# Kernel tuning notes

Measured on AMD Instinct MI355X. Metric: run time of the kernel, lower is better.

The kernel has to match this reference:

```python
import jax, jax.numpy as jnp
import numpy as np


def _layer_norm(x, w, b, eps=1e-5):
    mu = jnp.mean(x, axis=-1, keepdims=True)
    var = jnp.mean((x - mu) ** 2, axis=-1, keepdims=True)
    return (x - mu) * jax.lax.rsqrt(var + eps) * w + b


def setup_inputs() -> dict:
    key = jax.random.key(0)
    ks = jax.random.split(key, 6)
    B, S, E, H = 4, 4096, 1024, 16
    dk = E // H            # = n_qubits_transformer = 64
    NQF = 64               # n_qubits_ffn
    x = jax.random.normal(ks[0], (B, S, E), jnp.float32)
    attn_q_params = jax.random.normal(ks[1], (dk, 3), jnp.float32)   # torch.randn init
    out_proj_w = jax.random.normal(ks[2], (E, E), jnp.float32) / np.float32(np.sqrt(E))
    out_proj_b = jnp.zeros((E,), jnp.float32)
    ffn_q_params = jax.random.normal(ks[3], (NQF, 3), jnp.float32)
    ffn_lin_w = jax.random.normal(ks[4], (E, NQF), jnp.float32) / np.float32(np.sqrt(NQF))
    ffn_lin_b = jnp.zeros((E,), jnp.float32)
    return {
        'x': x,
        'attn_q_params': attn_q_params,
        'out_proj_w': out_proj_w,
        'out_proj_b': out_proj_b,
        'ffn_q_params': ffn_q_params,
        'ffn_lin_w': ffn_lin_w,
        'ffn_lin_b': ffn_lin_b,
        'norm1_w': jnp.ones((E,), jnp.float32),
        'norm1_b': jnp.zeros((E,), jnp.float32),
        'norm2_w': jnp.ones((E,), jnp.float32),
        'norm2_b': jnp.zeros((E,), jnp.float32),
    }


def reference(x, attn_q_params, out_proj_w, out_proj_b,
              ffn_q_params, ffn_lin_w, ffn_lin_b,
              norm1_w, norm1_b, norm2_w, norm2_b):
    # Closed form: <Z> = cos(x + a) * cos(b); Rz does not affect <Z>.
    B, S, E = x.shape
    dk = attn_q_params.shape[0]
    H = E // dk
    # ---- quantum multi-head attention (shared QHead params across heads) ----
    heads = x.reshape(B, S, H, dk)                                   # bshd
    z = jnp.cos(heads + attn_q_params[:, 0]) * jnp.cos(attn_q_params[:, 1])
    attn_out = z.reshape(B, S, E) @ out_proj_w.T + out_proj_b
    x1 = _layer_norm(x + attn_out, norm1_w, norm1_b)                 # dropout = identity (eval)
    # ---- quantum feed-forward: encoder uses first n_qubits_ffn features ----
    nq = ffn_q_params.shape[0]
    q = jnp.cos(x1[..., :nq] + ffn_q_params[:, 0]) * jnp.cos(ffn_q_params[:, 1])
    ffn_out = q @ ffn_lin_w.T + ffn_lin_b
    return _layer_norm(x1 + ffn_out, norm2_w, norm2_b)
```

## Files before the change

### kernel.cpp

```cpp
#include <hip/hip_runtime.h>
#include <math.h>

typedef __attribute__((ext_vector_type(8))) short short8;
typedef __attribute__((ext_vector_type(4))) float f32x4;
typedef unsigned short u16;

#define DEV static __device__ __forceinline__

DEV u16 f2bf(float f) {
  union { float f; unsigned u; } v; v.f = f;
  unsigned r = v.u + 0x7FFFu + ((v.u >> 16) & 1u);
  return (u16)(r >> 16);
}
DEV float bf2f(u16 u) {
  union { unsigned u; float f; } v; v.u = ((unsigned)u) << 16;
  return v.f;
}

__global__ __launch_bounds__(256) void k_conv(const float* __restrict__ W,
                                              const float* __restrict__ Wf,
                                              u16* __restrict__ Wb,
                                              u16* __restrict__ Wfb) {
  int i = (blockIdx.x * 256 + threadIdx.x) * 4;
  const int NW = 1024 * 1024;
  if (i < NW) {
    float4 v = *(const float4*)(W + i);
    ushort4 o = {f2bf(v.x), f2bf(v.y), f2bf(v.z), f2bf(v.w)};
    *(ushort4*)(Wb + i) = o;
  } else {
    int j = i - NW;
    float4 v = *(const float4*)(Wf + j);
    ushort4 o = {f2bf(v.x), f2bf(v.y), f2bf(v.z), f2bf(v.w)};
    *(ushort4*)(Wfb + j) = o;
  }
}

__global__ __launch_bounds__(256) void k_zenc(const float* __restrict__ x,
                                              const float* __restrict__ qp,
                                              u16* __restrict__ z) {
  __shared__ float a0[64], c1[64];
  int t = threadIdx.x;
  if (t < 64) { a0[t] = qp[t * 3]; c1[t] = cosf(qp[t * 3 + 1]); }
  __syncthreads();
  size_t i = ((size_t)blockIdx.x * 256 + t) * 4;
  float4 xv = *(const float4*)(x + i);
  int d = (int)(i & 63);
  ushort4 o;
  o.x = f2bf(cosf(xv.x + a0[d + 0]) * c1[d + 0]);
  o.y = f2bf(cosf(xv.y + a0[d + 1]) * c1[d + 1]);
  o.z = f2bf(cosf(xv.z + a0[d + 2]) * c1[d + 2]);
  o.w = f2bf(cosf(xv.w + a0[d + 3]) * c1[d + 3]);
  *(ushort4*)(z + i) = o;
}

__global__ __launch_bounds__(256) void k_gemm(const u16* __restrict__ Z,
                                              const u16* __restrict__ Wb,
                                              const float* __restrict__ x,
                                              const float* __restrict__ bias,
                                              float* __restrict__ Y) {
  constexpr int K = 1024, N = 1024;
  __shared__ __attribute__((aligned(16))) u16 As[2][128 * 32];
  __shared__ __attribute__((aligned(16))) u16 Bs[2][128 * 32];
  int bid = blockIdx.x;
  int wg = (bid & 7) * 128 + (bid >> 3);
  int mt = wg >> 3, nt = wg & 7;
  int m0 = mt * 128, n0 = nt * 128;
  int t = threadIdx.x, lane = t & 63, wv = t >> 6;
  int wr = wv >> 1, wc = wv & 1;

  int srow = t >> 2;
  int scol = (t & 3) * 8;
  const u16* gA = Z + (size_t)(m0 + srow) * K + scol;
  const u16* gB = Wb + (size_t)(n0 + srow) * K + scol;
  int lbase = wv * 512;

  f32x4 acc[4][4];
#pragma unroll
  for (int i = 0; i < 4; ++i)
#pragma unroll
    for (int j = 0; j < 4; ++j) acc[i][j] = (f32x4){0.f, 0.f, 0.f, 0.f};

  auto stage = [&](int buf, int kt) {
    const u16* ga = gA + kt * 32;
    const u16* gb = gB + kt * 32;
#pragma unroll
    for (int j = 0; j < 2; ++j) {
      __builtin_amdgcn_global_load_lds(
          (const __attribute__((address_space(1))) unsigned int*)(ga + (size_t)j * 64 * K),
          (__attribute__((address_space(3))) unsigned int*)&As[buf][j * 2048 + lbase],
          16, 0, 0);
      __builtin_amdgcn_global_load_lds(
          (const __attribute__((address_space(1))) unsigned int*)(gb + (size_t)j * 64 * K),
          (__attribute__((address_space(3))) unsigned int*)&Bs[buf][j * 2048 + lbase],
          16, 0, 0);
    }
  };

  stage(0, 0);
  int kof = (lane >> 4) * 8;
  int arow = wr * 64 + (lane & 15);
  int brow = wc * 64 + (lane & 15);
  int cur = 0;
  for (int kt = 0; kt < K / 32; ++kt) {
    __syncthreads();
    if (kt + 1 < K / 32) stage(cur ^ 1, kt + 1);
    short8 av[4], bv[4];
#pragma unroll
    for (int mi = 0; mi < 4; ++mi)
      av[mi] = *(const short8*)&As[cur][(arow + mi * 16) * 32 + kof];
#pragma unroll
    for (int ni = 0; ni < 4; ++ni)
      bv[ni] = *(const short8*)&Bs[cur][(brow + ni * 16) * 32 + kof];
#pragma unroll
    for (int mi = 0; mi < 4; ++mi)
#pragma unroll
      for (int ni = 0; ni < 4; ++ni)
        acc[mi][ni] = __builtin_amdgcn_mfma_f32_16x16x32_bf16(av[mi], bv[ni], acc[mi][ni], 0, 0, 0);
    cur ^= 1;
  }
  int r0 = m0 + wr * 64 + (lane >> 4) * 4;
  int c0 = n0 + wc * 64 + (lane & 15);
#pragma unroll
  for (int mi = 0; mi < 4; ++mi) {
#pragma unroll
    for (int ni = 0; ni < 4; ++ni) {
      int col = c0 + ni * 16;
      float bcol = bias[col];
#pragma unroll
      for (int r = 0; r < 4; ++r) {
        size_t idx = (size_t)(r0 + mi * 16 + r) * N + col;
        Y[idx] = acc[mi][ni][r] + x[idx] + bcol;
      }
    }
  }
}

__global__ __launch_bounds__(256) void k_ln1(const float* __restrict__ Y,
                                             const float* __restrict__ w1,
                                             const float* __restrict__ b1,
                                             const float* __restrict__ fqp,
                                             u16* __restrict__ X1,
                                             u16* __restrict__ Q) {
  int t = threadIdx.x, lane = t & 63, wv = t >> 6;
  int row = blockIdx.x * 4 + wv;
  const float* yr = Y + (size_t)row * 1024;
  float4 v[4];
  float s = 0.f, s2 = 0.f;
#pragma unroll
  for (int j = 0; j < 4; ++j) {
    v[j] = *(const float4*)(yr + j * 256 + lane * 4);
    s += v[j].x + v[j].y + v[j].z + v[j].w;
    s2 += v[j].x * v[j].x + v[j].y * v[j].y + v[j].z * v[j].z + v[j].w * v[j].w;
  }
#pragma unroll
  for (int m = 1; m < 64; m <<= 1) { s += __shfl_xor(s, m, 64); s2 += __shfl_xor(s2, m, 64); }
  float mu = s * (1.f / 1024.f);
  float var = s2 * (1.f / 1024.f) - mu * mu;
  float rs = rsqrtf(var + 1e-5f);
  float q0[4];
#pragma unroll
  for (int j = 0; j < 4; ++j) {
    int col = j * 256 + lane * 4;
    float4 wv4 = *(const float4*)(w1 + col);
    float4 bv4 = *(const float4*)(b1 + col);
    float o0 = (v[j].x - mu) * rs * wv4.x + bv4.x;
    float o1 = (v[j].y - mu) * rs * wv4.y + bv4.y;
    float o2 = (v[j].z - mu) * rs * wv4.z + bv4.z;
    float o3 = (v[j].w - mu) * rs * wv4.w + bv4.w;
    ushort4 o = {f2bf(o0), f2bf(o1), f2bf(o2), f2bf(o3)};
    *(ushort4*)(X1 + (size_t)row * 1024 + col) = o;
    if (j == 0) { q0[0] = o0; q0[1] = o1; q0[2] = o2; q0[3] = o3; }
  }
  if (lane < 16) {
    ushort4 qo;
    u16* qs = (u16*)&qo;
#pragma unroll
    for (int c = 0; c < 4; ++c) {
      int col = lane * 4 + c;
      qs[c] = f2bf(cosf(q0[c] + fqp[col * 3]) * cosf(fqp[col * 3 + 1]));
    }
    *(ushort4*)(Q + (size_t)row * 64 + lane * 4) = qo;
  }
}

__global__ __launch_bounds__(256) void k_ffn(const u16* __restrict__ X1,
                                             const u16* __restrict__ Q,
                                             const u16* __restrict__ Wfb,
                                             const float* __restrict__ fb,
                                             const float* __restrict__ w2,
                                             const float* __restrict__ b2,
                                             float* __restrict__ out) {
  __shared__ float t2[16][1024];
  int t = threadIdx.x, lane = t & 63, wv = t >> 6;
  int m0 = blockIdx.x * 16;
  int kof = (lane >> 4) * 8;
  const short8 a0v = *(const short8*)&Q[(size_t)(m0 + (lane & 15)) * 64 + kof];
  const short8 a1v = *(const short8*)&Q[(size_t)(m0 + (lane & 15)) * 64 + 32 + kof];
  int nbase = wv * 256;
#pragma unroll
  for (int ni = 0; ni < 16; ++ni) {
    int n = nbase + ni * 16 + (lane & 15);
    short8 b0 = *(const short8*)&Wfb[(size_t)n * 64 + kof];
    short8 b1 = *(const short8*)&Wfb[(size_t)n * 64 + 32 + kof];
    f32x4 acc = (f32x4){0.f, 0.f, 0.f, 0.f};
    acc = __builtin_amdgcn_mfma_f32_16x16x32_bf16(a0v, b0, acc, 0, 0, 0);
    acc = __builtin_amdgcn_mfma_f32_16x16x32_bf16(a1v, b1, acc, 0, 0, 0);
#pragma unroll
    for (int r = 0; r < 4; ++r) t2[(lane >> 4) * 4 + r][n] = acc[r];
  }
  __syncthreads();
  for (int rr = 0; rr < 4; ++rr) {
    int row = wv * 4 + rr;
    size_t grow = (size_t)(m0 + row) * 1024;
    float vv[16];
    float s = 0.f, s2 = 0.f;
#pragma unroll
    for (int j = 0; j < 16; ++j) {
      int col = j * 64 + lane;
      float val = bf2f(X1[grow + col]) + t2[row][col] + fb[col];
      vv[j] = val; s += val; s2 += val * val;
    }
#pragma unroll
    for (int m = 1; m < 64; m <<= 1) { s += __shfl_xor(s, m, 64); s2 += __shfl_xor(s2, m, 64); }
    float mu = s * (1.f / 1024.f);
    float var = s2 * (1.f / 1024.f) - mu * mu;
    float rs = rsqrtf(var + 1e-5f);
#pragma unroll
    for (int j = 0; j < 16; ++j) {
      int col = j * 64 + lane;
      out[grow + col] = (vv[j] - mu) * rs * w2[col] + b2[col];
    }
  }
}

extern "C" void kernel_launch(void* const* d_in, const int* in_sizes, int n_in,
                              void* d_out, int out_size, void* d_ws, size_t ws_size,
                              hipStream_t stream) {
  const float* x   = (const float*)d_in[0];
  const float* aqp = (const float*)d_in[1];
  const float* opw = (const float*)d_in[2];
  const float* opb = (const float*)d_in[3];
  const float* fqp = (const float*)d_in[4];
  const float* flw = (const float*)d_in[5];
  const float* flb = (const float*)d_in[6];
  const float* n1w = (const float*)d_in[7];
  const float* n1b = (const float*)d_in[8];
  const float* n2w = (const float*)d_in[9];
  const float* n2b = (const float*)d_in[10];
  float* Y = (float*)d_out;

  char* ws = (char*)d_ws;
  u16* zbuf = (u16*)(ws + 0);
  u16* Wb   = (u16*)(ws + 33554432);
  u16* Wfb  = (u16*)(ws + 35651584);
  u16* Qb   = (u16*)(ws + 35782656);

  k_conv<<<1088, 256, 0, stream>>>(opw, flw, Wb, Wfb);
  k_zenc<<<16384, 256, 0, stream>>>(x, aqp, zbuf);
  k_gemm<<<1024, 256, 0, stream>>>(zbuf, Wb, x, opb, Y);
  k_ln1<<<4096, 256, 0, stream>>>(Y, n1w, n1b, fqp, zbuf , Qb);
  k_ffn<<<1024, 256, 0, stream>>>(zbuf, Qb, Wfb, flb, n2w, n2b, Y);
}
```

Before: 138.9 us.

## Fuse output-projection GEMM with LayerNorm1 using full-row tiles per block

Replaces the separate GEMM and LayerNorm1 kernels with one kernel. Each 512-thread block computes a 64-row by full-1024-column output tile, so row statistics can be reduced in registers and shared memory. It then writes bf16 X1 and the FFN encoder inputs directly, removing the fp32 intermediate write and re-read. The cost is one large block per CU with about 130KB of LDS for the double-buffered B tile and 128 accumulator registers per lane. That leaves low occupancy, weaker latency hiding, and a whole-block synchronization on every k-step.

```diff
diff --git a/kernel.cpp b/kernel.cpp
--- a/kernel.cpp
+++ b/kernel.cpp
@@ -53,133 +53,143 @@
   *(ushort4*)(z + i) = o;
 }
 
-__global__ __launch_bounds__(256) void k_gemm(const u16* __restrict__ Z,
-                                              const u16* __restrict__ Wb,
-                                              const float* __restrict__ x,
-                                              const float* __restrict__ bias,
-                                              float* __restrict__ Y) {
-  constexpr int K = 1024, N = 1024;
-  __shared__ __attribute__((aligned(16))) u16 As[2][128 * 32];
-  __shared__ __attribute__((aligned(16))) u16 Bs[2][128 * 32];
-  int bid = blockIdx.x;
-  int wg = (bid & 7) * 128 + (bid >> 3);
-  int mt = wg >> 3, nt = wg & 7;
-  int m0 = mt * 128, n0 = nt * 128;
+__global__ __launch_bounds__(512) void k_gemm_ln1(
+    const u16* __restrict__ Z, const u16* __restrict__ Wb,
+    const float* __restrict__ x, const float* __restrict__ opb,
+    const float* __restrict__ w1, const float* __restrict__ b1,
+    const float* __restrict__ fqp,
+    u16* __restrict__ X1, u16* __restrict__ Q) {
+  constexpr int K = 1024;
+  __shared__ __attribute__((aligned(16))) u16 As[2][64 * 32];
+  __shared__ __attribute__((aligned(16))) u16 Bs[2][1024 * 32];
+  __shared__ float redS[64][8];
+  __shared__ float redQ[64][8];
+  __shared__ float muF[64], rsF[64];
+
   int t = threadIdx.x, lane = t & 63, wv = t >> 6;
-  int wr = wv >> 1, wc = wv & 1;
-
-  int srow = t >> 2;
-  int scol = (t & 3) * 8;
-  const u16* gA = Z + (size_t)(m0 + srow) * K + scol;
-  const u16* gB = Wb + (size_t)(n0 + srow) * K + scol;
-  int lbase = wv * 512;
-
-  f32x4 acc[4][4];
-#pragma unroll
-  for (int i = 0; i < 4; ++i)
-#pragma unroll
-    for (int j = 0; j < 4; ++j) acc[i][j] = (f32x4){0.f, 0.f, 0.f, 0.f};
+  int m0 = blockIdx.x * 64;
+
+  const u16* gA = Z + (size_t)(m0 + (t >> 2)) * K + (t & 3) * 8;
+  const u16* gB = Wb + (size_t)(t >> 2) * K + (t & 3) * 8;
 
   auto stage = [&](int buf, int kt) {
-    const u16* ga = gA + kt * 32;
-    const u16* gb = gB + kt * 32;
-#pragma unroll
-    for (int j = 0; j < 2; ++j) {
+    int ko = kt * 32;
+    if (t < 256) {
       __builtin_amdgcn_global_load_lds(
-          (const __attribute__((address_space(1))) unsigned int*)(ga + (size_t)j * 64 * K),
-          (__attribute__((address_space(3))) unsigned int*)&As[buf][j * 2048 + lbase],
+          (const __attribute__((address_space(1))) unsigned int*)(gA + ko),
+          (__attribute__((address_space(3))) unsigned int*)&As[buf][wv * 512],
           16, 0, 0);
+    }
+#pragma unroll
+    for (int j = 0; j < 8; ++j) {
       __builtin_amdgcn_global_load_lds(
-          (const __attribute__((address_space(1))) unsigned int*)(gb + (size_t)j * 64 * K),
-          (__attribute__((address_space(3))) unsigned int*)&Bs[buf][j * 2048 + lbase],
+          (const __attribute__((address_space(1))) unsigned int*)(gB + (size_t)j * 128 * K + ko),
+          (__attribute__((address_space(3))) unsigned int*)&Bs[buf][j * 4096 + wv * 512],
           16, 0, 0);
     }
   };
 
+  f32x4 acc[4][8];
+#pragma unroll
+  for (int m = 0; m < 4; ++m)
+#pragma unroll
+    for (int n = 0; n < 8; ++n) acc[m][n] = (f32x4){0.f, 0.f, 0.f, 0.f};
+
   stage(0, 0);
+  int cur = 0;
   int kof = (lane >> 4) * 8;
-  int arow = wr * 64 + (lane & 15);
-  int brow = wc * 64 + (lane & 15);
-  int cur = 0;
+  int cl = lane & 15;
   for (int kt = 0; kt < K / 32; ++kt) {
     __syncthreads();
     if (kt + 1 < K / 32) stage(cur ^ 1, kt + 1);
-    short8 av[4], bv[4];
-#pragma unroll
-    for (int mi = 0; mi < 4; ++mi)
-      av[mi] = *(const short8*)&As[cur][(arow + mi * 16) * 32 + kof];
-#pragma unroll
-    for (int ni = 0; ni < 4; ++ni)
-      bv[ni] = *(const short8*)&Bs[cur][(brow + ni * 16) * 32 + kof];
-#pragma unroll
-    for (int mi = 0; mi < 4; ++mi)
-#pragma unroll
-      for (int ni = 0; ni < 4; ++ni)
-        acc[mi][ni] = __builtin_amdgcn_mfma_f32_16x16x32_bf16(av[mi], bv[ni], acc[mi][ni], 0, 0, 0);
+    short8 av[4], bv[8];
+#pragma unroll
+    for (int m = 0; m < 4; ++m)
+      av[m] = *(const short8*)&As[cur][(m * 16 + cl) * 32 + kof];
+#pragma unroll
+    for (int n = 0; n < 8; ++n)
+      bv[n] = *(const short8*)&Bs[cur][(wv * 128 + n * 16 + cl) * 32 + kof];
+#pragma unroll
+    for (int m = 0; m < 4; ++m)
+#pragma unroll
+      for (int n = 0; n < 8; ++n)
+        acc[m][n] = __builtin_amdgcn_mfma_f32_16x16x32_bf16(av[m], bv[n], acc[m][n], 0, 0, 0);
     cur ^= 1;
   }
-  int r0 = m0 + wr * 64 + (lane >> 4) * 4;
-  int c0 = n0 + wc * 64 + (lane & 15);
-#pragma unroll
-  for (int mi = 0; mi < 4; ++mi) {
-#pragma unroll
-    for (int ni = 0; ni < 4; ++ni) {
-      int col = c0 + ni * 16;
-      float bcol = bias[col];
+
+  int rbase = (lane >> 4) * 4;
+  float w1c[8], b1c[8];
+#pragma unroll
+  for (int n = 0; n < 8; ++n) {
+    int col = wv * 128 + n * 16 + cl;
+    w1c[n] = w1[col];
+    b1c[n] = b1[col];
+  }
+  float rowS[16], rowQ2[16];
+#pragma unroll
+  for (int i = 0; i < 16; ++i) { rowS[i] = 0.f; rowQ2[i] = 0.f; }
+#pragma unroll
+  for (int m = 0; m < 4; ++m) {
+#pragma unroll
+    for (int n = 0; n < 8; ++n) {
+      int col = wv * 128 + n * 16 + cl;
+      float bias = opb[col];
 #pragma unroll
       for (int r = 0; r < 4; ++r) {
-        size_t idx = (size_t)(r0 + mi * 16 + r) * N + col;
-        Y[idx] = acc[mi][ni][r] + x[idx] + bcol;
+        int row = m * 16 + rbase + r;
+        float v = acc[m][n][r] + x[(size_t)(m0 + row) * 1024 + col] + bias;
+        acc[m][n][r] = v;
+        rowS[m * 4 + r] += v;
+        rowQ2[m * 4 + r] += v * v;
       }
     }
   }
-}
-
-__global__ __launch_bounds__(256) void k_ln1(const float* __restrict__ Y,
-                                             const float* __restrict__ w1,
-                                             const float* __restrict__ b1,
-                                             const float* __restrict__ fqp,
-                                             u16* __restrict__ X1,
-                                             u16* __restrict__ Q) {
-  int t = threadIdx.x, lane = t & 63, wv = t >> 6;
-  int row = blockIdx.x * 4 + wv;
-  const float* yr = Y + (size_t)row * 1024;
-  float4 v[4];
-  float s = 0.f, s2 = 0.f;
-#pragma unroll
-  for (int j = 0; j < 4; ++j) {
-    v[j] = *(const float4*)(yr + j * 256 + lane * 4);
-    s += v[j].x + v[j].y + v[j].z + v[j].w;
-    s2 += v[j].x * v[j].x + v[j].y * v[j].y + v[j].z * v[j].z + v[j].w * v[j].w;
-  }
-#pragma unroll
-  for (int m = 1; m < 64; m <<= 1) { s += __shfl_xor(s, m, 64); s2 += __shfl_xor(s2, m, 64); }
-  float mu = s * (1.f / 1024.f);
-  float var = s2 * (1.f / 1024.f) - mu * mu;
-  float rs = rsqrtf(var + 1e-5f);
-  float q0[4];
-#pragma unroll
-  for (int j = 0; j < 4; ++j) {
-    int col = j * 256 + lane * 4;
-    float4 wv4 = *(const float4*)(w1 + col);
-    float4 bv4 = *(const float4*)(b1 + col);
-    float o0 = (v[j].x - mu) * rs * wv4.x + bv4.x;
-    float o1 = (v[j].y - mu) * rs * wv4.y + bv4.y;
-    float o2 = (v[j].z - mu) * rs * wv4.z + bv4.z;
-    float o3 = (v[j].w - mu) * rs * wv4.w + bv4.w;
-    ushort4 o = {f2bf(o0), f2bf(o1), f2bf(o2), f2bf(o3)};
-    *(ushort4*)(X1 + (size_t)row * 1024 + col) = o;
-    if (j == 0) { q0[0] = o0; q0[1] = o1; q0[2] = o2; q0[3] = o3; }
-  }
-  if (lane < 16) {
-    ushort4 qo;
-    u16* qs = (u16*)&qo;
-#pragma unroll
-    for (int c = 0; c < 4; ++c) {
-      int col = lane * 4 + c;
-      qs[c] = f2bf(cosf(q0[c] + fqp[col * 3]) * cosf(fqp[col * 3 + 1]));
-    }
-    *(ushort4*)(Q + (size_t)row * 64 + lane * 4) = qo;
+#pragma unroll
+  for (int i = 0; i < 16; ++i) {
+#pragma unroll
+    for (int msk = 1; msk < 16; msk <<= 1) {
+      rowS[i] += __shfl_xor(rowS[i], msk, 64);
+      rowQ2[i] += __shfl_xor(rowQ2[i], msk, 64);
+    }
+  }
+  if (cl == 0) {
+#pragma unroll
+    for (int m = 0; m < 4; ++m)
+#pragma unroll
+      for (int r = 0; r < 4; ++r) {
+        int row = m * 16 + rbase + r;
+        redS[row][wv] = rowS[m * 4 + r];
+        redQ[row][wv] = rowQ2[m * 4 + r];
+      }
+  }
+  __syncthreads();
+  if (t < 64) {
+    float s = 0.f, q = 0.f;
+#pragma unroll
+    for (int w = 0; w < 8; ++w) { s += redS[t][w]; q += redQ[t][w]; }
+    float mu = s * (1.f / 1024.f);
+    float var = q * (1.f / 1024.f) - mu * mu;
+    muF[t] = mu;
+    rsF[t] = rsqrtf(var + 1e-5f);
+  }
+  __syncthreads();
+#pragma unroll
+  for (int m = 0; m < 4; ++m) {
+#pragma unroll
+    for (int r = 0; r < 4; ++r) {
+      int row = m * 16 + rbase + r;
+      float mu = muF[row], rs = rsF[row];
+#pragma unroll
+      for (int n = 0; n < 8; ++n) {
+        int col = wv * 128 + n * 16 + cl;
+        float x1 = (acc[m][n][r] - mu) * rs * w1c[n] + b1c[n];
+        X1[(size_t)(m0 + row) * 1024 + col] = f2bf(x1);
+        if (wv == 0 && n < 4) {
+          float qv = cosf(x1 + fqp[col * 3]) * cosf(fqp[col * 3 + 1]);
+          Q[(size_t)(m0 + row) * 64 + col] = f2bf(qv);
+        }
+      }
+    }
   }
 }
 
@@ -247,7 +257,7 @@
   const float* n1b = (const float*)d_in[8];
   const float* n2w = (const float*)d_in[9];
   const float* n2b = (const float*)d_in[10];
-  float* Y = (float*)d_out;
+  float* out = (float*)d_out;
 
   char* ws = (char*)d_ws;
   u16* zbuf = (u16*)(ws + 0);
@@ -257,7 +267,7 @@
 
   k_conv<<<1088, 256, 0, stream>>>(opw, flw, Wb, Wfb);
   k_zenc<<<16384, 256, 0, stream>>>(x, aqp, zbuf);
-  k_gemm<<<1024, 256, 0, stream>>>(zbuf, Wb, x, opb, Y);
-  k_ln1<<<4096, 256, 0, stream>>>(Y, n1w, n1b, fqp, zbuf , Qb);
-  k_ffn<<<1024, 256, 0, stream>>>(zbuf, Qb, Wfb, flb, n2w, n2b, Y);
-}
+  k_gemm_ln1<<<256, 512, 0, stream>>>(zbuf, Wb, x, opb, n1w, n1b, fqp,
+                                      zbuf , Qb);
+  k_ffn<<<1024, 256, 0, stream>>>(zbuf, Qb, Wfb, flb, n2w, n2b, out);
+}
```

Result: slower. 449.8 us (+223.9%).

## Fuse LayerNorm row statistics into GEMM epilogue, store bf16 intermediate, swizzle LDS

Applied to the files above, without the earlier changes.

The GEMM epilogue now reduces per-row sums and sums of squares across lanes and writes partial stats per column tile. It stores the pre-norm activations as bf16 instead of fp32. The LN1 kernel then reads only the bf16 row plus 16 partial stats, which halves its traffic and drops its reduction pass. The GEMM also XOR-swizzles the LDS k-block layout to cut bank conflicts. This adds epilogue shuffles and an extra bf16 rounding of the pre-norm values before normalization.

```diff
diff --git a/kernel.cpp b/kernel.cpp
--- a/kernel.cpp
+++ b/kernel.cpp
@@ -56,8 +56,9 @@
 __global__ __launch_bounds__(256) void k_gemm(const u16* __restrict__ Z,
                                               const u16* __restrict__ Wb,
                                               const float* __restrict__ x,
-                                              const float* __restrict__ bias,
-                                              float* __restrict__ Y) {
+                                              const float* __restrict__ opb,
+                                              u16* __restrict__ Ybf,
+                                              float2* __restrict__ stats) {
   constexpr int K = 1024, N = 1024;
   __shared__ __attribute__((aligned(16))) u16 As[2][128 * 32];
   __shared__ __attribute__((aligned(16))) u16 Bs[2][128 * 32];
@@ -68,10 +69,9 @@
   int t = threadIdx.x, lane = t & 63, wv = t >> 6;
   int wr = wv >> 1, wc = wv & 1;
 
-  int srow = t >> 2;
-  int scol = (t & 3) * 8;
-  const u16* gA = Z + (size_t)(m0 + srow) * K + scol;
-  const u16* gB = Wb + (size_t)(n0 + srow) * K + scol;
+  int kb_log = (t & 3) ^ ((t >> 3) & 3);
+  const u16* gA = Z + (size_t)(m0 + (t >> 2)) * K + kb_log * 8;
+  const u16* gB = Wb + (size_t)(n0 + (t >> 2)) * K + kb_log * 8;
   int lbase = wv * 512;
 
   f32x4 acc[4][4];
@@ -97,9 +97,10 @@
   };
 
   stage(0, 0);
-  int kof = (lane >> 4) * 8;
-  int arow = wr * 64 + (lane & 15);
-  int brow = wc * 64 + (lane & 15);
+  int cl = lane & 15;
+  int kofs = ((lane >> 4) ^ ((lane >> 1) & 3)) * 8;
+  int arow = wr * 64 + cl;
+  int brow = wc * 64 + cl;
   int cur = 0;
   for (int kt = 0; kt < K / 32; ++kt) {
     __syncthreads();
@@ -107,10 +108,10 @@
     short8 av[4], bv[4];
 #pragma unroll
     for (int mi = 0; mi < 4; ++mi)
-      av[mi] = *(const short8*)&As[cur][(arow + mi * 16) * 32 + kof];
+      av[mi] = *(const short8*)&As[cur][(arow + mi * 16) * 32 + kofs];
 #pragma unroll
     for (int ni = 0; ni < 4; ++ni)
-      bv[ni] = *(const short8*)&Bs[cur][(brow + ni * 16) * 32 + kof];
+      bv[ni] = *(const short8*)&Bs[cur][(brow + ni * 16) * 32 + kofs];
 #pragma unroll
     for (int mi = 0; mi < 4; ++mi)
 #pragma unroll
@@ -118,24 +119,50 @@
         acc[mi][ni] = __builtin_amdgcn_mfma_f32_16x16x32_bf16(av[mi], bv[ni], acc[mi][ni], 0, 0, 0);
     cur ^= 1;
   }
+
   int r0 = m0 + wr * 64 + (lane >> 4) * 4;
-  int c0 = n0 + wc * 64 + (lane & 15);
+  int c0 = n0 + wc * 64 + cl;
+  float rowS[16], rowQ2[16];
+#pragma unroll
+  for (int i = 0; i < 16; ++i) { rowS[i] = 0.f; rowQ2[i] = 0.f; }
 #pragma unroll
   for (int mi = 0; mi < 4; ++mi) {
 #pragma unroll
     for (int ni = 0; ni < 4; ++ni) {
       int col = c0 + ni * 16;
-      float bcol = bias[col];
+      float bcol = opb[col];
 #pragma unroll
       for (int r = 0; r < 4; ++r) {
         size_t idx = (size_t)(r0 + mi * 16 + r) * N + col;
-        Y[idx] = acc[mi][ni][r] + x[idx] + bcol;
+        float v = acc[mi][ni][r] + x[idx] + bcol;
+        Ybf[idx] = f2bf(v);
+        rowS[mi * 4 + r] += v;
+        rowQ2[mi * 4 + r] += v * v;
       }
     }
   }
-}
-
-__global__ __launch_bounds__(256) void k_ln1(const float* __restrict__ Y,
+#pragma unroll
+  for (int i = 0; i < 16; ++i) {
+#pragma unroll
+    for (int msk = 1; msk < 16; msk <<= 1) {
+      rowS[i] += __shfl_xor(rowS[i], msk, 64);
+      rowQ2[i] += __shfl_xor(rowQ2[i], msk, 64);
+    }
+  }
+  if (cl == 0) {
+#pragma unroll
+    for (int mi = 0; mi < 4; ++mi)
+#pragma unroll
+      for (int r = 0; r < 4; ++r) {
+        int rg = r0 + mi * 16 + r;
+        stats[(size_t)rg * 16 + nt * 2 + wc] =
+            make_float2(rowS[mi * 4 + r], rowQ2[mi * 4 + r]);
+      }
+  }
+}
+
+__global__ __launch_bounds__(256) void k_ln1(const u16* __restrict__ Ybf,
+                                             const float2* __restrict__ stats,
                                              const float* __restrict__ w1,
                                              const float* __restrict__ b1,
                                              const float* __restrict__ fqp,
@@ -143,43 +170,45 @@
                                              u16* __restrict__ Q) {
   int t = threadIdx.x, lane = t & 63, wv = t >> 6;
   int row = blockIdx.x * 4 + wv;
-  const float* yr = Y + (size_t)row * 1024;
-  float4 v[4];
-  float s = 0.f, s2 = 0.f;
-#pragma unroll
-  for (int j = 0; j < 4; ++j) {
-    v[j] = *(const float4*)(yr + j * 256 + lane * 4);
-    s += v[j].x + v[j].y + v[j].z + v[j].w;
-    s2 += v[j].x * v[j].x + v[j].y * v[j].y + v[j].z * v[j].z + v[j].w * v[j].w;
-  }
-#pragma unroll
-  for (int m = 1; m < 64; m <<= 1) { s += __shfl_xor(s, m, 64); s2 += __shfl_xor(s2, m, 64); }
+  float2 st = stats[(size_t)row * 16 + (lane & 15)];
+  float s = st.x, s2 = st.y;
+#pragma unroll
+  for (int msk = 1; msk < 16; msk <<= 1) {
+    s += __shfl_xor(s, msk, 64);
+    s2 += __shfl_xor(s2, msk, 64);
+  }
   float mu = s * (1.f / 1024.f);
   float var = s2 * (1.f / 1024.f) - mu * mu;
   float rs = rsqrtf(var + 1e-5f);
-  float q0[4];
-#pragma unroll
-  for (int j = 0; j < 4; ++j) {
-    int col = j * 256 + lane * 4;
-    float4 wv4 = *(const float4*)(w1 + col);
-    float4 bv4 = *(const float4*)(b1 + col);
-    float o0 = (v[j].x - mu) * rs * wv4.x + bv4.x;
-    float o1 = (v[j].y - mu) * rs * wv4.y + bv4.y;
-    float o2 = (v[j].z - mu) * rs * wv4.z + bv4.z;
-    float o3 = (v[j].w - mu) * rs * wv4.w + bv4.w;
-    ushort4 o = {f2bf(o0), f2bf(o1), f2bf(o2), f2bf(o3)};
-    *(ushort4*)(X1 + (size_t)row * 1024 + col) = o;
-    if (j == 0) { q0[0] = o0; q0[1] = o1; q0[2] = o2; q0[3] = o3; }
-  }
-  if (lane < 16) {
-    ushort4 qo;
-    u16* qs = (u16*)&qo;
-#pragma unroll
-    for (int c = 0; c < 4; ++c) {
-      int col = lane * 4 + c;
-      qs[c] = f2bf(cosf(q0[c] + fqp[col * 3]) * cosf(fqp[col * 3 + 1]));
-    }
-    *(ushort4*)(Q + (size_t)row * 64 + lane * 4) = qo;
+
+  size_t base = (size_t)row * 1024 + lane * 16;
+  short8 y0 = *(const short8*)&Ybf[base];
+  short8 y1 = *(const short8*)&Ybf[base + 8];
+  float x1v[16];
+#pragma unroll
+  for (int j = 0; j < 8; ++j) x1v[j] = bf2f((u16)y0[j]);
+#pragma unroll
+  for (int j = 0; j < 8; ++j) x1v[8 + j] = bf2f((u16)y1[j]);
+  int col0 = lane * 16;
+#pragma unroll
+  for (int j = 0; j < 16; ++j)
+    x1v[j] = (x1v[j] - mu) * rs * w1[col0 + j] + b1[col0 + j];
+  short8 o0, o1;
+#pragma unroll
+  for (int j = 0; j < 8; ++j) { o0[j] = (short)f2bf(x1v[j]); o1[j] = (short)f2bf(x1v[8 + j]); }
+  *(short8*)&X1[base] = o0;
+  *(short8*)&X1[base + 8] = o1;
+
+  if (lane < 4) {
+    short8 q0, q1;
+#pragma unroll
+    for (int j = 0; j < 16; ++j) {
+      int c = col0 + j;
+      float qv = cosf(x1v[j] + fqp[c * 3]) * cosf(fqp[c * 3 + 1]);
+      if (j < 8) q0[j] = (short)f2bf(qv); else q1[j - 8] = (short)f2bf(qv);
+    }
+    *(short8*)&Q[(size_t)row * 64 + col0] = q0;
+    *(short8*)&Q[(size_t)row * 64 + col0 + 8] = q1;
   }
 }
 
@@ -247,7 +276,7 @@
   const float* n1b = (const float*)d_in[8];
   const float* n2w = (const float*)d_in[9];
   const float* n2b = (const float*)d_in[10];
-  float* Y = (float*)d_out;
+  float* out = (float*)d_out;
 
   char* ws = (char*)d_ws;
   u16* zbuf = (u16*)(ws + 0);
@@ -255,9 +284,12 @@
   u16* Wfb  = (u16*)(ws + 35651584);
   u16* Qb   = (u16*)(ws + 35782656);
 
+  u16* Ybf = (u16*)d_out;
+  float2* stats = (float2*)((char*)d_out + 33554432);
+
   k_conv<<<1088, 256, 0, stream>>>(opw, flw, Wb, Wfb);
   k_zenc<<<16384, 256, 0, stream>>>(x, aqp, zbuf);
-  k_gemm<<<1024, 256, 0, stream>>>(zbuf, Wb, x, opb, Y);
-  k_ln1<<<4096, 256, 0, stream>>>(Y, n1w, n1b, fqp, zbuf , Qb);
-  k_ffn<<<1024, 256, 0, stream>>>(zbuf, Qb, Wfb, flb, n2w, n2b, Y);
-}
+  k_gemm<<<1024, 256, 0, stream>>>(zbuf, Wb, x, opb, Ybf, stats);
+  k_ln1<<<4096, 256, 0, stream>>>(Ybf, stats, n1w, n1b, fqp, zbuf , Qb);
+  k_ffn<<<1024, 256, 0, stream>>>(zbuf, Qb, Wfb, flb, n2w, n2b, out);
+}
```

Measured after the change: 200.7 us. 44.5% more time.
